# Optimization experiments

Measured on AMD Instinct MI355X. Metric: run time of the kernel, lower is better.

## Reference

```python
import jax, jax.numpy as jnp
import numpy as np

B, S, D, H = 32, 512, 768, 12
HD = D // H
FF = 4 * D
EPS = 1e-5


def layernorm(x, g, b):
    mu = jnp.mean(x, axis=-1, keepdims=True)
    var = jnp.mean(jnp.square(x - mu), axis=-1, keepdims=True)
    return (x - mu) * jax.lax.rsqrt(var + EPS) * g + b


def setup_inputs() -> dict:
    key = jax.random.key(0)
    ks = jax.random.split(key, 10)
    s = 0.02
    return {
        "x": jax.random.normal(ks[0], (B, S, D), jnp.float32),
        "edge_bias": jax.random.normal(ks[1], (H, S, S), jnp.float32) * s,
        "ln1_g": jnp.ones((D,), jnp.float32),
        "ln1_b": jnp.zeros((D,), jnp.float32),
        "qkv_w": jax.random.normal(ks[2], (3 * D, D), jnp.float32) * s,
        "qkv_b": jnp.zeros((3 * D,), jnp.float32),
        "proj_w": jax.random.normal(ks[3], (D, D), jnp.float32) * s,
        "proj_b": jnp.zeros((D,), jnp.float32),
        "ln2_g": jnp.ones((D,), jnp.float32),
        "ln2_b": jnp.zeros((D,), jnp.float32),
        "fc1_w": jax.random.normal(ks[4], (FF, D), jnp.float32) * s,
        "fc1_b": jnp.zeros((FF,), jnp.float32),
        "fc2_w": jax.random.normal(ks[5], (D, FF), jnp.float32) * s,
        "fc2_b": jnp.zeros((D,), jnp.float32),
    }


def reference(x, edge_bias, ln1_g, ln1_b, qkv_w, qkv_b, proj_w, proj_b,
              ln2_g, ln2_b, fc1_w, fc1_b, fc2_w, fc2_b):
    shortcut = x
    xn = layernorm(x, ln1_g, ln1_b)
    # qkv: [B,S,3D] -> [3,B,H,S,HD]
    qkv = (xn @ qkv_w.T + qkv_b).reshape(B, S, 3, H, HD).transpose(2, 0, 3, 1, 4)
    q, k, v = qkv[0], qkv[1], qkv[2]
    q = q * (HD ** -0.5)
    attn = jnp.einsum('bhqd,bhkd->bhqk', q, k) + edge_bias[None]
    attn = jax.nn.softmax(attn, axis=-1)
    o = jnp.einsum('bhqk,bhkd->bhqd', attn, v)
    o = o.transpose(0, 2, 1, 3).reshape(B, S, D)
    o = o @ proj_w.T + proj_b
    x = shortcut + o
    h = layernorm(x, ln2_g, ln2_b)
    h = jax.nn.gelu(h @ fc1_w.T + fc1_b, approximate=False)
    h = h @ fc2_w.T + fc2_b
    return x + h
```

## Files before the change

### kernel.cpp

```cpp
#include <hip/hip_runtime.h>

typedef unsigned short u16;
typedef unsigned int u32;
typedef float f32x4 __attribute__((ext_vector_type(4)));
typedef __bf16 bf16x8 __attribute__((ext_vector_type(8)));

__device__ __forceinline__ u16 f2bf(float f) {
  u32 u = __float_as_uint(f);
  u += 0x7fffu + ((u >> 16) & 1u);
  return (u16)(u >> 16);
}

__device__ __forceinline__ float bf2f(u16 v) {
  return __uint_as_float((u32)v << 16);
}

__device__ __forceinline__ void gload16(const u16* g, u16* l) {
  __builtin_amdgcn_global_load_lds(
      (__attribute__((address_space(1))) void*)(u16*)g,
      (__attribute__((address_space(3))) void*)l, 16, 0, 0);
}

__global__ __launch_bounds__(256) void cvt_bf16(const float* __restrict__ in,
                                                u16* __restrict__ o, int n4) {
  int i = blockIdx.x * 256 + threadIdx.x;
  if (i >= n4) return;
  float4 f = reinterpret_cast<const float4*>(in)[i];
  u32 lo = (u32)f2bf(f.x) | ((u32)f2bf(f.y) << 16);
  u32 hi = (u32)f2bf(f.z) | ((u32)f2bf(f.w) << 16);
  reinterpret_cast<uint2*>(o)[i] = make_uint2(lo, hi);
}

__global__ __launch_bounds__(256) void ln_bf16(const float* __restrict__ x,
                                               const float* __restrict__ g,
                                               const float* __restrict__ b,
                                               u16* __restrict__ o) {
  const int row = blockIdx.x;
  const int t = threadIdx.x;
  const float* xr = x + (size_t)row * 768;
  float a0 = xr[t], a1 = xr[t + 256], a2 = xr[t + 512];
  float s = a0 + a1 + a2;
  float ss = a0 * a0 + a1 * a1 + a2 * a2;
#pragma unroll
  for (int m = 1; m < 64; m <<= 1) {
    s += __shfl_xor(s, m);
    ss += __shfl_xor(ss, m);
  }
  __shared__ float sb[8];
  if ((t & 63) == 0) { sb[t >> 6] = s; sb[4 + (t >> 6)] = ss; }
  __syncthreads();
  s = sb[0] + sb[1] + sb[2] + sb[3];
  ss = sb[4] + sb[5] + sb[6] + sb[7];
  const float mu = s * (1.0f / 768.0f);
  const float var = ss * (1.0f / 768.0f) - mu * mu;
  const float rs = rsqrtf(var + 1e-5f);
  u16* orow = o + (size_t)row * 768;
  orow[t]       = f2bf((a0 - mu) * rs * g[t] + b[t]);
  orow[t + 256] = f2bf((a1 - mu) * rs * g[t + 256] + b[t + 256]);
  orow[t + 512] = f2bf((a2 - mu) * rs * g[t + 512] + b[t + 512]);
}

enum { EPI_QKV = 0, EPI_PROJ = 1, EPI_GELU = 2, EPI_OUT = 3 };

template <int EPI>
__global__ __launch_bounds__(512, 2) void gemm_bt(
    const u16* __restrict__ A, const u16* __restrict__ W,
    const float* __restrict__ bias, const float* __restrict__ res,
    float* __restrict__ outf, u16* __restrict__ outb,
    u16* __restrict__ outq, u16* __restrict__ outk, u16* __restrict__ outv,
    int M, int N, int K) {
  __shared__ u16 SA[4 * 8192];
  __shared__ u16 SB[4 * 8192];
  const int tid = threadIdx.x;
  const int wid = tid >> 6, l = tid & 63;
  const int wm = wid >> 2, wn = wid & 3;
  const int lg = l >> 4, lc = l & 15;

  const u32 nbn = gridDim.x;
  const u32 orig = blockIdx.y * nbn + blockIdx.x;
  const u32 cpx = (nbn * gridDim.y) >> 3;
  const u32 wgid = (orig & 7) * cpx + (orig >> 3);
  const int bn = wgid % nbn;
  const int bm = wgid / nbn;

  const u16* Ab = A + (size_t)(bm * 256) * K;
  const u16* Wb = W + (size_t)(bn * 256) * K;

  const int lrow = wid * 16 + (l >> 2);
  const int ksrc = ((l & 3) ^ ((l >> 3) & 3)) * 8;

  const int sg = (lg ^ ((lc >> 1) & 3)) << 3;

  f32x4 acc[8][4] = {};

  const int NU = K >> 5;

#define STAGE(u)                                                            \
  {                                                                         \
    const int slot_ = (u) & 3;                                              \
    const int ku_ = (u) * 32;                                               \
    gload16(Ab + (size_t)lrow * K + ku_ + ksrc, &SA[slot_ * 8192 + wid * 512]); \
    gload16(Ab + (size_t)(128 + lrow) * K + ku_ + ksrc,                     \
            &SA[slot_ * 8192 + 4096 + wid * 512]);                          \
    gload16(Wb + (size_t)lrow * K + ku_ + ksrc, &SB[slot_ * 8192 + wid * 512]); \
    gload16(Wb + (size_t)(128 + lrow) * K + ku_ + ksrc,                     \
            &SB[slot_ * 8192 + 4096 + wid * 512]);                          \
  }

  STAGE(0);
  STAGE(1);
  STAGE(2);
  asm volatile("s_waitcnt vmcnt(8)" ::: "memory");
  __builtin_amdgcn_s_barrier();

  for (int u = 0; u < NU; ++u) {
    const u16* sa = &SA[(u & 3) * 8192];
    const u16* sb = &SB[(u & 3) * 8192];
    bf16x8 af[8], bf[4];
#pragma unroll
    for (int mi = 0; mi < 8; ++mi)
      af[mi] = *reinterpret_cast<const bf16x8*>(&sa[(wm * 128 + mi * 16 + lc) * 32 + sg]);
#pragma unroll
    for (int ni = 0; ni < 4; ++ni)
      bf[ni] = *reinterpret_cast<const bf16x8*>(&sb[(wn * 64 + ni * 16 + lc) * 32 + sg]);
    if (u + 3 < NU) STAGE(u + 3);
    __builtin_amdgcn_s_barrier();
    __builtin_amdgcn_s_setprio(1);
#pragma unroll
    for (int mi = 0; mi < 8; ++mi)
#pragma unroll
      for (int ni = 0; ni < 4; ++ni)
        acc[mi][ni] = __builtin_amdgcn_mfma_f32_16x16x32_bf16(af[mi], bf[ni], acc[mi][ni], 0, 0, 0);
    __builtin_amdgcn_s_setprio(0);
    if (u + 3 < NU) {
      asm volatile("s_waitcnt vmcnt(8)" ::: "memory");
    } else if (u + 2 < NU) {
      asm volatile("s_waitcnt vmcnt(4)" ::: "memory");
    } else if (u + 1 < NU) {
      asm volatile("s_waitcnt vmcnt(0)" ::: "memory");
    }
    __builtin_amdgcn_s_barrier();
  }
#undef STAGE

  const int rbase = bm * 256 + wm * 128;
  const int cbase = bn * 256 + wn * 64;
#pragma unroll
  for (int mi = 0; mi < 8; ++mi) {
#pragma unroll
    for (int ni = 0; ni < 4; ++ni) {
#pragma unroll
      for (int r = 0; r < 4; ++r) {
        const int i = rbase + mi * 16 + lg * 4 + r;
        const int j = cbase + ni * 16 + lc;
        float v = acc[mi][ni][r] + bias[j];
        if constexpr (EPI == EPI_QKV) {
          const int t = j / 768;
          const int rr = j - t * 768;
          const int h = rr >> 6, hd = rr & 63;
          const int bb = i >> 9, ssi = i & 511;
          if (t == 0) {
            outq[((size_t)(bb * 12 + h) * 512 + ssi) * 64 + hd] = f2bf(v * 0.125f);
          } else if (t == 1) {
            outk[((size_t)(bb * 12 + h) * 512 + ssi) * 64 + hd] = f2bf(v);
          } else {
            outv[((size_t)(bb * 12 + h) * 64 + hd) * 512 + ssi] = f2bf(v);
          }
        } else if constexpr (EPI == EPI_PROJ) {
          outf[(size_t)i * 768 + j] = v + res[(size_t)i * 768 + j];
        } else if constexpr (EPI == EPI_GELU) {
          float gl = 0.5f * v * (1.0f + erff(v * 0.70710678118654752f));
          outb[(size_t)i * 3072 + j] = f2bf(gl);
        } else {
          outf[(size_t)i * 768 + j] = v + res[(size_t)i * 768 + j];
        }
      }
    }
  }
}

__global__ __launch_bounds__(256) void attn_fwd(const u16* __restrict__ q,
                                                const u16* __restrict__ k,
                                                const u16* __restrict__ vt,
                                                const u16* __restrict__ ebb,
                                                u16* __restrict__ o) {
  __shared__ u16 Ks[128 * 64];
  __shared__ u16 Vs[64 * 128];
  __shared__ u16 Bs[64 * 128];
  __shared__ u16 P[4 * 1024];
  const int tid = threadIdx.x;
  const int w = tid >> 6, l = tid & 63;
  const int lg = l >> 4, lc = l & 15;
  const int xcd = blockIdx.x & 7;
  const int wg = xcd * 384 + (blockIdx.x >> 3);
  const int qt = wg & 7;
  const int b = (wg >> 3) & 31;
  const int h = wg >> 8;
  const int bh = b * 12 + h;
  const int q0 = qt * 64;
  const u16* qp = q + (size_t)bh * 512 * 64;
  const u16* kp = k + (size_t)bh * 512 * 64;
  const u16* vtp = vt + (size_t)bh * 64 * 512;
  const u16* ep = ebb + (size_t)h * 262144 + (size_t)q0 * 512;

  bf16x8 aq[2];
#pragma unroll
  for (int kk = 0; kk < 2; ++kk)
    aq[kk] = *reinterpret_cast<const bf16x8*>(qp + (q0 + w * 16 + lc) * 64 + kk * 32 + lg * 8);

  float m[4], lsum[4];
  f32x4 oa[4] = {};
#pragma unroll
  for (int r = 0; r < 4; ++r) { m[r] = -1e30f; lsum[r] = 0.f; }

  const int krow_l = l >> 3;
  const int kgr = ((l & 7) ^ (l >> 3)) << 3;
  const int vrow_l = l >> 4;
  const int vswz = 4 * (w & 1) + (l >> 4);
  const int vgr = (((l & 15) ^ vswz)) << 3;
  const int bgr = (l & 15) << 3;
  char* Pw = (char*)&P[w * 1024];

  for (int kc = 0; kc < 4; ++kc) {
    const int kb = kc * 128;
    __syncthreads();
#pragma unroll
    for (int i = 0; i < 4; ++i) {
      const int grp = i * 4 + w;
      gload16(kp + (size_t)(kb + grp * 8 + krow_l) * 64 + kgr, &Ks[grp * 512]);
      gload16(vtp + (size_t)(grp * 4 + vrow_l) * 512 + kb + vgr, &Vs[grp * 512]);
      gload16(ep + (size_t)(grp * 4 + vrow_l) * 512 + kb + bgr, &Bs[grp * 512]);
    }
    __syncthreads();

    f32x4 s[8] = {};
#pragma unroll
    for (int kt = 0; kt < 8; ++kt) {
      const int kbyte = (kt * 16 + lc) * 128;
      const int sw = lc & 7;
      bf16x8 b0 = *reinterpret_cast<const bf16x8*>((const char*)Ks + kbyte + ((lg ^ sw) << 4));
      bf16x8 b1 = *reinterpret_cast<const bf16x8*>((const char*)Ks + kbyte + (((4 + lg) ^ sw) << 4));
      s[kt] = __builtin_amdgcn_mfma_f32_16x16x32_bf16(aq[0], b0, s[kt], 0, 0, 0);
      s[kt] = __builtin_amdgcn_mfma_f32_16x16x32_bf16(aq[1], b1, s[kt], 0, 0, 0);
    }
#pragma unroll
    for (int kt = 0; kt < 8; ++kt)
#pragma unroll
      for (int r = 0; r < 4; ++r)
        s[kt][r] += bf2f(Bs[(w * 16 + lg * 4 + r) * 128 + kt * 16 + lc]);
#pragma unroll
    for (int r = 0; r < 4; ++r) {
      float mc = s[0][r];
#pragma unroll
      for (int kt = 1; kt < 8; ++kt) mc = fmaxf(mc, s[kt][r]);
      mc = fmaxf(mc, __shfl_xor(mc, 1));
      mc = fmaxf(mc, __shfl_xor(mc, 2));
      mc = fmaxf(mc, __shfl_xor(mc, 4));
      mc = fmaxf(mc, __shfl_xor(mc, 8));
      const float mn = fmaxf(m[r], mc);
      const float al = __expf(m[r] - mn);
      m[r] = mn;
      float sum = 0.f;
#pragma unroll
      for (int kt = 0; kt < 8; ++kt) {
        float pv = __expf(s[kt][r] - mn);
        s[kt][r] = pv;
        sum += pv;
      }
      sum += __shfl_xor(sum, 1);
      sum += __shfl_xor(sum, 2);
      sum += __shfl_xor(sum, 4);
      sum += __shfl_xor(sum, 8);
      lsum[r] = lsum[r] * al + sum;
#pragma unroll
      for (int ni = 0; ni < 4; ++ni) oa[ni][r] *= al;
    }
#pragma unroll
    for (int kt = 0; kt < 8; ++kt)
#pragma unroll
      for (int r = 0; r < 4; ++r) {
        const int row = lg * 4 + r;
        int byte = (row << 8) + ((kt * 16 + lc) << 1);
        byte ^= (row & 7) << 4;
        *reinterpret_cast<u16*>(Pw + byte) = f2bf(s[kt][r]);
      }
#pragma unroll
    for (int ks = 0; ks < 4; ++ks) {
      int pbyte = (lc << 8) + ks * 64 + lg * 16;
      pbyte ^= (lc & 7) << 4;
      bf16x8 pa = *reinterpret_cast<const bf16x8*>(Pw + pbyte);
#pragma unroll
      for (int ni = 0; ni < 4; ++ni) {
        const int vbyte = (ni * 16 + lc) * 256 + (((ks * 4 + lg) ^ (lc & 7)) << 4);
        bf16x8 bv = *reinterpret_cast<const bf16x8*>((const char*)Vs + vbyte);
        oa[ni] = __builtin_amdgcn_mfma_f32_16x16x32_bf16(pa, bv, oa[ni], 0, 0, 0);
      }
    }
  }

  float inv[4];
#pragma unroll
  for (int r = 0; r < 4; ++r) inv[r] = 1.0f / lsum[r];
  u16* op = o + ((size_t)(b * 512 + q0 + w * 16)) * 768 + h * 64;
#pragma unroll
  for (int ni = 0; ni < 4; ++ni)
#pragma unroll
    for (int r = 0; r < 4; ++r)
      op[(size_t)(lg * 4 + r) * 768 + ni * 16 + lc] = f2bf(oa[ni][r] * inv[r]);
}

extern "C" void kernel_launch(void* const* d_in, const int* in_sizes, int n_in,
                              void* d_out, int out_size, void* d_ws, size_t ws_size,
                              hipStream_t stream) {
  const float* x     = (const float*)d_in[0];
  const float* ebias = (const float*)d_in[1];
  const float* ln1g  = (const float*)d_in[2];
  const float* ln1b  = (const float*)d_in[3];
  const float* qkvw  = (const float*)d_in[4];
  const float* qkvb  = (const float*)d_in[5];
  const float* projw = (const float*)d_in[6];
  const float* projb = (const float*)d_in[7];
  const float* ln2g  = (const float*)d_in[8];
  const float* ln2b  = (const float*)d_in[9];
  const float* fc1w  = (const float*)d_in[10];
  const float* fc1b  = (const float*)d_in[11];
  const float* fc2w  = (const float*)d_in[12];
  const float* fc2b  = (const float*)d_in[13];
  float* out = (float*)d_out;

  char* p = (char*)d_ws;
  const size_t ACT = (size_t)16384 * 768 * 2;
  u16* xnb = (u16*)(p);
  u16* qb  = (u16*)(p + ACT);
  u16* kb  = (u16*)(p + 2 * ACT);
  u16* vb  = (u16*)(p + 3 * ACT);
  u16* ffb = (u16*)(p + 4 * ACT);
  u16* ebb = (u16*)(p + 4 * ACT);
  float* x2 = (float*)(p + 4 * ACT + (size_t)16384 * 3072 * 2);
  char* wz = p + 4 * ACT + (size_t)16384 * 3072 * 2 + (size_t)16384 * 768 * 4;
  u16* wq  = (u16*)wz;
  u16* wp  = wq + (size_t)2304 * 768;
  u16* wf1 = wp + (size_t)768 * 768;
  u16* wf2 = wf1 + (size_t)3072 * 768;

  cvt_bf16<<<1728, 256, 0, stream>>>(qkvw, wq, 442368);
  cvt_bf16<<<576, 256, 0, stream>>>(projw, wp, 147456);
  cvt_bf16<<<2304, 256, 0, stream>>>(fc1w, wf1, 589824);
  cvt_bf16<<<2304, 256, 0, stream>>>(fc2w, wf2, 589824);
  cvt_bf16<<<3072, 256, 0, stream>>>(ebias, ebb, 786432);

  ln_bf16<<<16384, 256, 0, stream>>>(x, ln1g, ln1b, xnb);

  gemm_bt<EPI_QKV><<<dim3(9, 64), 512, 0, stream>>>(
      xnb, wq, qkvb, nullptr, nullptr, nullptr, qb, kb, vb, 16384, 2304, 768);

  attn_fwd<<<3072, 256, 0, stream>>>(qb, kb, vb, ebb, xnb);

  gemm_bt<EPI_PROJ><<<dim3(3, 64), 512, 0, stream>>>(
      xnb, wp, projb, x, x2, nullptr, nullptr, nullptr, nullptr, 16384, 768, 768);

  ln_bf16<<<16384, 256, 0, stream>>>(x2, ln2g, ln2b, kb);

  gemm_bt<EPI_GELU><<<dim3(12, 64), 512, 0, stream>>>(
      kb, wf1, fc1b, nullptr, nullptr, ffb, nullptr, nullptr, nullptr, 16384, 3072, 768);

  gemm_bt<EPI_OUT><<<dim3(3, 64), 512, 0, stream>>>(
      ffb, wf2, fc2b, x2, out, nullptr, nullptr, nullptr, nullptr, 16384, 768, 3072);
}
```

Measured before the change: 574.2 us.

## Store GEMM operands in K-sliced panel layout for contiguous tile loads

Weights and activations feeding the GEMMs (LN outputs, attention output, GELU output) are now written in a [K/32][rows][32] panel layout instead of row-major. Each 32-wide K step of a 256-row tile then becomes one contiguous 16 KB block, replacing strided row reads. The change also simplifies per-stage address arithmetic. The cost is scattered 2-byte stores in the LN, attention and GELU epilogues, which may coalesce poorly.

```diff
diff --git a/kernel.cpp b/kernel.cpp
--- a/kernel.cpp
+++ b/kernel.cpp
@@ -29,6 +29,23 @@
   u32 lo = (u32)f2bf(f.x) | ((u32)f2bf(f.y) << 16);
   u32 hi = (u32)f2bf(f.z) | ((u32)f2bf(f.w) << 16);
   reinterpret_cast<uint2*>(o)[i] = make_uint2(lo, hi);
+}
+
+__global__ __launch_bounds__(256) void cvt_w_pack(const float* __restrict__ in,
+                                                  u16* __restrict__ o, int N, int K) {
+  int i = blockIdx.x * 256 + threadIdx.x;
+  const int ng = K >> 3;
+  if (i >= N * ng) return;
+  const int n = i / ng;
+  const int k = (i - n * ng) * 8;
+  const float4 f0 = reinterpret_cast<const float4*>(in + (size_t)n * K + k)[0];
+  const float4 f1 = reinterpret_cast<const float4*>(in + (size_t)n * K + k)[1];
+  u32 p0 = (u32)f2bf(f0.x) | ((u32)f2bf(f0.y) << 16);
+  u32 p1 = (u32)f2bf(f0.z) | ((u32)f2bf(f0.w) << 16);
+  u32 p2 = (u32)f2bf(f1.x) | ((u32)f2bf(f1.y) << 16);
+  u32 p3 = (u32)f2bf(f1.z) | ((u32)f2bf(f1.w) << 16);
+  u16* dst = o + ((size_t)(k >> 5) * N + n) * 32 + (k & 31);
+  reinterpret_cast<uint4*>(dst)[0] = make_uint4(p0, p1, p2, p3);
 }
 
 __global__ __launch_bounds__(256) void ln_bf16(const float* __restrict__ x,
@@ -54,10 +71,13 @@
   const float mu = s * (1.0f / 768.0f);
   const float var = ss * (1.0f / 768.0f) - mu * mu;
   const float rs = rsqrtf(var + 1e-5f);
-  u16* orow = o + (size_t)row * 768;
-  orow[t]       = f2bf((a0 - mu) * rs * g[t] + b[t]);
-  orow[t + 256] = f2bf((a1 - mu) * rs * g[t + 256] + b[t + 256]);
-  orow[t + 512] = f2bf((a2 - mu) * rs * g[t + 512] + b[t + 512]);
+#pragma unroll
+  for (int c = 0; c < 3; ++c) {
+    const int col = t + c * 256;
+    const float a = (c == 0) ? a0 : (c == 1) ? a1 : a2;
+    o[((size_t)(col >> 5) * 16384 + row) * 32 + (col & 31)] =
+        f2bf((a - mu) * rs * g[col] + b[col]);
+  }
 }
 
 enum { EPI_QKV = 0, EPI_PROJ = 1, EPI_GELU = 2, EPI_OUT = 3 };
@@ -83,11 +103,12 @@
   const int bn = wgid % nbn;
   const int bm = wgid / nbn;
 
-  const u16* Ab = A + (size_t)(bm * 256) * K;
-  const u16* Wb = W + (size_t)(bn * 256) * K;
-
-  const int lrow = wid * 16 + (l >> 2);
-  const int ksrc = ((l & 3) ^ ((l >> 3) & 3)) * 8;
+  const size_t Msl = (size_t)M * 32;
+  const size_t Nsl = (size_t)N * 32;
+  const size_t lane_a = (size_t)(bm * 256 + wid * 16 + (l >> 2)) * 32 +
+                        (((l & 3) ^ ((l >> 3) & 3)) << 3);
+  const size_t lane_w = (size_t)(bn * 256 + wid * 16 + (l >> 2)) * 32 +
+                        (((l & 3) ^ ((l >> 3) & 3)) << 3);
 
   const int sg = (lg ^ ((lc >> 1) & 3)) << 3;
 
@@ -95,16 +116,15 @@
 
   const int NU = K >> 5;
 
-#define STAGE(u)                                                            \
-  {                                                                         \
-    const int slot_ = (u) & 3;                                              \
-    const int ku_ = (u) * 32;                                               \
-    gload16(Ab + (size_t)lrow * K + ku_ + ksrc, &SA[slot_ * 8192 + wid * 512]); \
-    gload16(Ab + (size_t)(128 + lrow) * K + ku_ + ksrc,                     \
-            &SA[slot_ * 8192 + 4096 + wid * 512]);                          \
-    gload16(Wb + (size_t)lrow * K + ku_ + ksrc, &SB[slot_ * 8192 + wid * 512]); \
-    gload16(Wb + (size_t)(128 + lrow) * K + ku_ + ksrc,                     \
-            &SB[slot_ * 8192 + 4096 + wid * 512]);                          \
+#define STAGE(u)                                                      \
+  {                                                                   \
+    const int slot_ = (u) & 3;                                        \
+    const u16* Au_ = A + (size_t)(u) * Msl + lane_a;                  \
+    const u16* Wu_ = W + (size_t)(u) * Nsl + lane_w;                  \
+    gload16(Au_, &SA[slot_ * 8192 + wid * 512]);                      \
+    gload16(Au_ + 4096, &SA[slot_ * 8192 + 4096 + wid * 512]);        \
+    gload16(Wu_, &SB[slot_ * 8192 + wid * 512]);                      \
+    gload16(Wu_ + 4096, &SB[slot_ * 8192 + 4096 + wid * 512]);        \
   }
 
   STAGE(0);
@@ -170,7 +190,7 @@
           outf[(size_t)i * 768 + j] = v + res[(size_t)i * 768 + j];
         } else if constexpr (EPI == EPI_GELU) {
           float gl = 0.5f * v * (1.0f + erff(v * 0.70710678118654752f));
-          outb[(size_t)i * 3072 + j] = f2bf(gl);
+          outb[((size_t)(j >> 5) * 16384 + i) * 32 + (j & 31)] = f2bf(gl);
         } else {
           outf[(size_t)i * 768 + j] = v + res[(size_t)i * 768 + j];
         }
@@ -301,12 +321,14 @@
   float inv[4];
 #pragma unroll
   for (int r = 0; r < 4; ++r) inv[r] = 1.0f / lsum[r];
-  u16* op = o + ((size_t)(b * 512 + q0 + w * 16)) * 768 + h * 64;
 #pragma unroll
   for (int ni = 0; ni < 4; ++ni)
 #pragma unroll
-    for (int r = 0; r < 4; ++r)
-      op[(size_t)(lg * 4 + r) * 768 + ni * 16 + lc] = f2bf(oa[ni][r] * inv[r]);
+    for (int r = 0; r < 4; ++r) {
+      const int i = b * 512 + q0 + w * 16 + lg * 4 + r;
+      const int j = h * 64 + ni * 16 + lc;
+      o[((size_t)(j >> 5) * 16384 + i) * 32 + (j & 31)] = f2bf(oa[ni][r] * inv[r]);
+    }
 }
 
 extern "C" void kernel_launch(void* const* d_in, const int* in_sizes, int n_in,
@@ -343,10 +365,10 @@
   u16* wf1 = wp + (size_t)768 * 768;
   u16* wf2 = wf1 + (size_t)3072 * 768;
 
-  cvt_bf16<<<1728, 256, 0, stream>>>(qkvw, wq, 442368);
-  cvt_bf16<<<576, 256, 0, stream>>>(projw, wp, 147456);
-  cvt_bf16<<<2304, 256, 0, stream>>>(fc1w, wf1, 589824);
-  cvt_bf16<<<2304, 256, 0, stream>>>(fc2w, wf2, 589824);
+  cvt_w_pack<<<864, 256, 0, stream>>>(qkvw, wq, 2304, 768);
+  cvt_w_pack<<<288, 256, 0, stream>>>(projw, wp, 768, 768);
+  cvt_w_pack<<<1152, 256, 0, stream>>>(fc1w, wf1, 3072, 768);
+  cvt_w_pack<<<1152, 256, 0, stream>>>(fc2w, wf2, 768, 3072);
   cvt_bf16<<<3072, 256, 0, stream>>>(ebias, ebb, 786432);
 
   ln_bf16<<<16384, 256, 0, stream>>>(x, ln1g, ln1b, xnb);
```

Measured after the change: 536.9 us. 6.5% less time.
